# Kernel optimization log

Hardware: AMD Instinct MI355X
Metric: run time of the kernel (lower is better)

## Reference

```python
import jax, jax.numpy as jnp
import numpy as np

C = 256

def setup_inputs() -> dict:
    key = jax.random.key(0)
    ks = jax.random.split(key, 9)
    B, H, W = 32, 32, 32
    s = C ** -0.5  # init scale for weights
    inputs = jax.random.normal(ks[0], (B, H, W, C), jnp.float32)
    Wq = jax.random.normal(ks[1], (C, C), jnp.float32) * s
    Wk = jax.random.normal(ks[2], (C, C), jnp.float32) * s
    Wv = jax.random.normal(ks[3], (C, C), jnp.float32) * s
    Wo = jax.random.normal(ks[4], (C, C), jnp.float32) * s
    bq = jnp.zeros((C,), jnp.float32)
    bk = jnp.zeros((C,), jnp.float32)
    bv = jnp.zeros((C,), jnp.float32)
    bo = jnp.zeros((C,), jnp.float32)
    return {"inputs": inputs, "Wq": Wq, "bq": bq, "Wk": Wk, "bk": bk,
            "Wv": Wv, "bv": bv, "Wo": Wo, "bo": bo}

def reference(inputs, Wq, bq, Wk, bk, Wv, bv, Wo, bo):
    B, H, W, c = inputs.shape
    scale = jnp.float32(c) ** -0.5
    x = inputs.reshape(B, H * W, c)           # 1x1 conv == per-pixel matmul
    q = x @ Wq + bq                           # [B, HW, C]
    k = x @ Wk + bk
    v = x @ Wv + bv
    scores = jnp.einsum('bnc,bmc->bnm', q, k) * scale  # [B, HW, HW]
    attn = jax.nn.softmax(scores, axis=-1)
    attended = jnp.einsum('bnm,bmc->bnc', attn, v)     # [B, HW, C]
    out = attended @ Wo + bo
    return out.reshape(B, H, W, c)
```

## Files before the change

kernel.cpp:

```cpp
#include <hip/hip_runtime.h>
#include <hip/hip_bf16.h>

typedef __bf16 bf16;
typedef __bf16 bf16x2 __attribute__((ext_vector_type(2)));
typedef __bf16 bf16x4 __attribute__((ext_vector_type(4)));
typedef __bf16 bf16x8 __attribute__((ext_vector_type(8)));
typedef float f32x4 __attribute__((ext_vector_type(4)));

#define SM_C 0.09016994374947424f

typedef __attribute__((address_space(1))) const void as1_void;
typedef __attribute__((address_space(3))) void as3_void;

__global__ __launch_bounds__(256) void transpose_w(
    const float* __restrict__ Wq, const float* __restrict__ Wk,
    const float* __restrict__ Wv, const float* __restrict__ Wo,
    bf16* __restrict__ Wt)
{
    __shared__ float T[32][33];
    const int bid = blockIdx.x;
    const int m = bid >> 6, tile = bid & 63;
    const int tn0 = (tile >> 3) * 32, tk0 = (tile & 7) * 32;
    const float* W = (m == 0) ? Wq : (m == 1) ? Wk : (m == 2) ? Wv : Wo;

    const int t = threadIdx.x;
    const int r = t >> 3, c4 = (t & 7) * 4;

    f32x4 v = *(const f32x4*)(W + (size_t)(tk0 + r) * 256 + tn0 + c4);
#pragma unroll
    for (int j = 0; j < 4; ++j) T[r][c4 + j] = v[j];
    __syncthreads();

    bf16x4 ov;
#pragma unroll
    for (int j = 0; j < 4; ++j) ov[j] = (bf16)T[c4 + j][r];
    *(bf16x4*)(Wt + (size_t)m * 65536 + (size_t)(tn0 + r) * 256 + tk0 + c4) = ov;
}

__global__ __launch_bounds__(256, 3) void qkv_gemm(
    const float* __restrict__ X, const bf16* __restrict__ Wt,
    const float* __restrict__ bq, const float* __restrict__ bk,
    const float* __restrict__ bv,
    bf16* __restrict__ Qo, bf16* __restrict__ Ko, bf16* __restrict__ Vto)
{
    __shared__ bf16 Xs[128 * 72];
    __shared__ bf16 Ws_[128 * 72];

    const int t    = threadIdx.x;
    const int lane = t & 63, wv = t >> 6;
    const int quad = lane >> 4, l16 = lane & 15;
    const int bm   = blockIdx.x;
    const int bn   = blockIdx.y;
    const int proj = bn >> 1;

    const bf16* W = Wt + (size_t)proj * 65536 + (size_t)(bn & 1) * 32768;
    const float* bias = (proj == 0) ? bq : (proj == 1) ? bk : bv;

    const int m0 = t >> 3;
    const int c0 = (t & 7) * 8;

    const f32x4 zero = {0.0f, 0.0f, 0.0f, 0.0f};
    f32x4 acc[2][8];
#pragma unroll
    for (int i = 0; i < 2; ++i)
#pragma unroll
        for (int j = 0; j < 8; ++j) acc[i][j] = zero;

    f32x4 xa[4], xb[4]; bf16x8 wp[4];
#pragma unroll
    for (int p = 0; p < 4; ++p) {
        const float* px = X + (size_t)(bm * 128 + m0 + p * 32) * 256 + c0;
        xa[p] = *(const f32x4*)px; xb[p] = *(const f32x4*)(px + 4);
        wp[p] = *(const bf16x8*)(W + (size_t)(m0 + p * 32) * 256 + c0);
    }

    for (int kt = 0; kt < 4; ++kt) {
#pragma unroll
        for (int p = 0; p < 4; ++p) {
            bf16x8 r;
#pragma unroll
            for (int j = 0; j < 4; ++j) { r[j] = (bf16)xa[p][j]; r[j + 4] = (bf16)xb[p][j]; }
            *(bf16x8*)(Xs + (m0 + p * 32) * 72 + c0) = r;
            *(bf16x8*)(Ws_ + (m0 + p * 32) * 72 + c0) = wp[p];
        }
        __syncthreads();

        if (kt < 3) {
#pragma unroll
            for (int p = 0; p < 4; ++p) {
                const float* px = X + (size_t)(bm * 128 + m0 + p * 32) * 256 + (kt + 1) * 64 + c0;
                xa[p] = *(const f32x4*)px; xb[p] = *(const f32x4*)(px + 4);
                wp[p] = *(const bf16x8*)(W + (size_t)(m0 + p * 32) * 256 + (kt + 1) * 64 + c0);
            }
        }

#pragma unroll
        for (int ks = 0; ks < 2; ++ks) {
            bf16x8 a[2], bb[8];
#pragma unroll
            for (int mt = 0; mt < 2; ++mt)
                a[mt] = *(const bf16x8*)(Xs + (wv * 32 + mt * 16 + l16) * 72 + ks * 32 + quad * 8);
#pragma unroll
            for (int nt = 0; nt < 8; ++nt)
                bb[nt] = *(const bf16x8*)(Ws_ + (nt * 16 + l16) * 72 + ks * 32 + quad * 8);
#pragma unroll
            for (int mt = 0; mt < 2; ++mt)
#pragma unroll
                for (int nt = 0; nt < 8; ++nt)
                    acc[mt][nt] = __builtin_amdgcn_mfma_f32_16x16x32_bf16(
                        a[mt], bb[nt], acc[mt][nt], 0, 0, 0);
        }
        __syncthreads();
    }

#pragma unroll
    for (int nt = 0; nt < 8; ++nt) {
        int col = (bn & 1) * 128 + nt * 16 + l16;
        float bvv = bias[col];
#pragma unroll
        for (int mt = 0; mt < 2; ++mt) {
            int grow0 = bm * 128 + wv * 32 + mt * 16 + quad * 4;
            if (proj == 2) {
                bf16x4 pk;
#pragma unroll
                for (int r = 0; r < 4; ++r) pk[r] = (bf16)(acc[mt][nt][r] + bvv);
                int b = grow0 >> 10, m = grow0 & 1023;
                *(bf16x4*)(Vto + (size_t)b * 262144 + (size_t)col * 1024 + m) = pk;
            } else {
                bf16* dst = (proj == 0) ? Qo : Ko;
#pragma unroll
                for (int r = 0; r < 4; ++r)
                    dst[(size_t)(grow0 + r) * 256 + col] = (bf16)(acc[mt][nt][r] + bvv);
            }
        }
    }
}

__global__ __launch_bounds__(512, 2) void flash_attn(
    const bf16* __restrict__ Qr, const bf16* __restrict__ K,
    const bf16* __restrict__ Vt, const bf16* __restrict__ Wo,
    const float* __restrict__ bo, float* __restrict__ out)
{
    __shared__ __align__(16) char smem[155648];

    const int t    = threadIdx.x;
    const int lane = t & 63, wv = t >> 6;
    const int quad = lane >> 4, l16 = lane & 15;
    const int g    = wv >> 2, wl = wv & 3;
    const int gt   = t & 255;
    const int b  = blockIdx.x;
    const int qt = blockIdx.y;

    char* const KsB = smem + g * 73728;
    char* const VsB = smem + g * 73728 + 32768;
    char* const Pb  = smem + 147456 + wv * 1024;
    const int psw = (l16 & 7) << 4;

    bf16x8 qf[2][8];
#pragma unroll
    for (int mt = 0; mt < 2; ++mt) {
        const bf16* qp = Qr + ((size_t)b * 1024 + qt * 128 + wl * 32 + mt * 16 + l16) * 256 + quad * 8;
#pragma unroll
        for (int ks = 0; ks < 8; ++ks)
            qf[mt][ks] = *(const bf16x8*)(qp + ks * 32);
    }

    const f32x4 zero = {0.0f, 0.0f, 0.0f, 0.0f};
    f32x4 o[2][16];
#pragma unroll
    for (int mt = 0; mt < 2; ++mt)
#pragma unroll
        for (int n = 0; n < 16; ++n) o[mt][n] = zero;
    float lst[2] = {0.f, 0.f};

    const int vc  = gt >> 1;
    const int vk8 = (gt & 1) * 8;
    bf16x8 vp[4];

    auto gloadK = [&](int T, int buf) {
#pragma unroll
        for (int p = 0; p < 4; ++p) {
            int chunk = wl * 4 + p;
            int row   = chunk * 2 + (lane >> 5);
            int w16   = (lane & 31) ^ (row & 7);
            const bf16* gsrc = K + ((size_t)b * 1024 + T * 32 + row) * 256 + w16 * 8;
            __builtin_amdgcn_global_load_lds((as1_void*)gsrc,
                (as3_void*)(KsB + buf * 16384 + chunk * 1024), 16, 0, 0);
        }
    };
    auto vload = [&](int T) {
#pragma unroll
        for (int p = 0; p < 4; ++p) {
            int c = vc + 128 * (p >> 1), k8 = vk8 + (p & 1) * 16;
            vp[p] = *(const bf16x8*)(Vt + (size_t)b * 262144 + (size_t)c * 1024 + T * 32 + k8);
        }
    };
    auto vcommit = [&](int buf) {
#pragma unroll
        for (int p = 0; p < 4; ++p) {
            int c = vc + 128 * (p >> 1), k8 = vk8 + (p & 1) * 16;
            *(bf16x8*)(VsB + buf * 20480 + c * 80 + k8 * 2) = vp[p];
        }
    };

    gloadK(g, 0);
    vload(g); vcommit(0); vload(g + 2);

    for (int i = 0; i < 16; ++i) {
        const int buf = i & 1;
        __syncthreads();

        if (i < 15) {
            gloadK(g + 2 * (i + 1), buf ^ 1);
            vcommit(buf ^ 1);
            if (i < 14) vload(g + 2 * (i + 2));
        }

        f32x4 s[2][2];
        s[0][0] = zero; s[0][1] = zero; s[1][0] = zero; s[1][1] = zero;
        const char* Kbuf = KsB + buf * 16384;
#pragma unroll
        for (int ks = 0; ks < 8; ++ks) {
#pragma unroll
            for (int n = 0; n < 2; ++n) {
                bf16x8 kb = *(const bf16x8*)(Kbuf + (n * 16 + l16) * 512 + ((ks * 64 + quad * 16) ^ psw));
                s[0][n] = __builtin_amdgcn_mfma_f32_16x16x32_bf16(kb, qf[0][ks], s[0][n], 0, 0, 0);
                s[1][n] = __builtin_amdgcn_mfma_f32_16x16x32_bf16(kb, qf[1][ks], s[1][n], 0, 0, 0);
            }
        }

        bf16x8 af[2];
#pragma unroll
        for (int mt = 0; mt < 2; ++mt) {
#pragma unroll
            for (int n = 0; n < 2; ++n) {
#pragma unroll
                for (int h = 0; h < 2; ++h) {
                    float p0 = __builtin_amdgcn_exp2f(s[mt][n][2 * h] * SM_C);
                    float p1 = __builtin_amdgcn_exp2f(s[mt][n][2 * h + 1] * SM_C);
                    lst[mt] += p0 + p1;
                    bf16x2 pk; pk[0] = (bf16)p0; pk[1] = (bf16)p1;
                    *(bf16x2*)(Pb + ((l16 * 64 + n * 32 + quad * 8 + h * 4) ^ psw)) = pk;
                }
            }
            af[mt] = *(const bf16x8*)(Pb + ((l16 * 64 + quad * 16) ^ psw));
        }

        const char* Vbuf = VsB + buf * 20480;
#pragma unroll
        for (int n = 0; n < 16; ++n) {
            bf16x8 vb = *(const bf16x8*)(Vbuf + (n * 16 + l16) * 80 + quad * 16);
            o[0][n] = __builtin_amdgcn_mfma_f32_16x16x32_bf16(af[0], vb, o[0][n], 0, 0, 0);
            o[1][n] = __builtin_amdgcn_mfma_f32_16x16x32_bf16(af[1], vb, o[1][n], 0, 0, 0);
        }
    }

    __syncthreads();

#pragma unroll
    for (int mt = 0; mt < 2; ++mt) {
        lst[mt] += __shfl_xor(lst[mt], 16, 64);
        lst[mt] += __shfl_xor(lst[mt], 32, 64);
    }

    float* const scr  = (float*)(smem + 67584);
    float* const lstS = (float*)(smem + 135168);
    bf16*  const Os   = (bf16*)smem;

    if (g == 1) {
        if (quad == 0) {
            lstS[wl * 32 + l16]      = lst[0];
            lstS[wl * 32 + 16 + l16] = lst[1];
        }
#pragma unroll
        for (int mt = 0; mt < 2; ++mt)
#pragma unroll
            for (int n = 0; n < 8; ++n)
                *(f32x4*)(scr + (size_t)(n * 16 + l16) * 132 + wl * 32 + mt * 16 + quad * 4) = o[mt][n];
    }
    __syncthreads();
    if (g == 0) {
        lst[0] += lstS[wl * 32 + l16];
        lst[1] += lstS[wl * 32 + 16 + l16];
#pragma unroll
        for (int mt = 0; mt < 2; ++mt)
#pragma unroll
            for (int n = 0; n < 8; ++n) {
                f32x4 m = *(const f32x4*)(scr + (size_t)(n * 16 + l16) * 132 + wl * 32 + mt * 16 + quad * 4);
                o[mt][n] += m;
            }
    }
    __syncthreads();
    if (g == 1) {
#pragma unroll
        for (int mt = 0; mt < 2; ++mt)
#pragma unroll
            for (int n = 8; n < 16; ++n)
                *(f32x4*)(scr + (size_t)((n - 8) * 16 + l16) * 132 + wl * 32 + mt * 16 + quad * 4) = o[mt][n];
    }
    __syncthreads();
    if (g == 0) {
#pragma unroll
        for (int mt = 0; mt < 2; ++mt)
#pragma unroll
            for (int n = 8; n < 16; ++n) {
                f32x4 m = *(const f32x4*)(scr + (size_t)((n - 8) * 16 + l16) * 132 + wl * 32 + mt * 16 + quad * 4);
                o[mt][n] += m;
            }
        float inv[2][4];
#pragma unroll
        for (int mt = 0; mt < 2; ++mt)
#pragma unroll
            for (int r = 0; r < 4; ++r)
                inv[mt][r] = 1.0f / __shfl(lst[mt], quad * 4 + r, 64);
#pragma unroll
        for (int mt = 0; mt < 2; ++mt)
#pragma unroll
            for (int n = 0; n < 16; ++n)
#pragma unroll
                for (int r = 0; r < 4; ++r)
                    Os[(size_t)(wl * 32 + mt * 16 + quad * 4 + r) * 264 + n * 16 + l16] =
                        (bf16)(o[mt][n][r] * inv[mt][r]);
    }
    __syncthreads();

    bf16* const Wos = (bf16*)(smem + 67584);
    const int rh = (wv & 1) * 64;
    const int nq = wv >> 1;
    const size_t orow0 = (size_t)b * 1024 + qt * 128 + rh;

#pragma unroll
    for (int h = 0; h < 2; ++h) {
        if (h) __syncthreads();
#pragma unroll
        for (int i = 0; i < 8; ++i) {
            int c = t + i * 512;
            int row = c >> 5, c8 = (c & 31) * 8;
            *(bf16x8*)(Wos + row * 264 + c8) =
                *(const bf16x8*)(Wo + (size_t)(h * 128 + row) * 256 + c8);
        }
        __syncthreads();

        f32x4 acc[4][2];
#pragma unroll
        for (int mt = 0; mt < 4; ++mt) { acc[mt][0] = zero; acc[mt][1] = zero; }

#pragma unroll
        for (int ks = 0; ks < 8; ++ks) {
            bf16x8 a[4], bb[2];
#pragma unroll
            for (int mt = 0; mt < 4; ++mt)
                a[mt] = *(const bf16x8*)(Os + (size_t)(rh + mt * 16 + l16) * 264 + ks * 32 + quad * 8);
#pragma unroll
            for (int nt = 0; nt < 2; ++nt)
                bb[nt] = *(const bf16x8*)(Wos + (nq * 32 + nt * 16 + l16) * 264 + ks * 32 + quad * 8);
#pragma unroll
            for (int mt = 0; mt < 4; ++mt)
#pragma unroll
                for (int nt = 0; nt < 2; ++nt)
                    acc[mt][nt] = __builtin_amdgcn_mfma_f32_16x16x32_bf16(
                        a[mt], bb[nt], acc[mt][nt], 0, 0, 0);
        }

#pragma unroll
        for (int nt = 0; nt < 2; ++nt) {
            int col = h * 128 + nq * 32 + nt * 16 + l16;
            float bvv = bo[col];
#pragma unroll
            for (int mt = 0; mt < 4; ++mt) {
#pragma unroll
                for (int r = 0; r < 4; ++r) {
                    size_t row = orow0 + mt * 16 + quad * 4 + r;
                    out[row * 256 + col] = acc[mt][nt][r] + bvv;
                }
            }
        }
    }
}

extern "C" void kernel_launch(void* const* d_in, const int* in_sizes, int n_in,
                              void* d_out, int out_size, void* d_ws, size_t ws_size,
                              hipStream_t stream)
{
    (void)in_sizes; (void)n_in; (void)out_size; (void)ws_size;
    const float* X  = (const float*)d_in[0];
    const float* Wq = (const float*)d_in[1];
    const float* bq = (const float*)d_in[2];
    const float* Wk = (const float*)d_in[3];
    const float* bk = (const float*)d_in[4];
    const float* Wv = (const float*)d_in[5];
    const float* bv = (const float*)d_in[6];
    const float* Wo = (const float*)d_in[7];
    const float* bo = (const float*)d_in[8];
    float* out = (float*)d_out;

    const size_t NTOK = (size_t)32768 * 256;

    bf16* Wt  = (bf16*)d_ws;
    bf16* Qw  = (bf16*)d_ws + 262144;
    bf16* Kw  = Qw + NTOK;
    bf16* Vtw = Kw + NTOK;

    transpose_w<<<256, 256, 0, stream>>>(Wq, Wk, Wv, Wo, Wt);
    qkv_gemm   <<<dim3(256, 6), 256, 0, stream>>>(X, Wt, bq, bk, bv, Qw, Kw, Vtw);
    flash_attn <<<dim3(32, 8),  512, 0, stream>>>(Qw, Kw, Vtw, Wt + 3 * 65536, bo, out);
}
```

Measured before the change: 199.7 us.

## Stage Q/K epilogue through LDS for coalesced stores and remap GEMM blocks per XCD

The QKV GEMM now writes Q and K tiles into shared memory first, then stores them to global memory as coalesced 16-byte vectors instead of scattered 2-byte writes. The grid becomes 1D, and block indices are remapped so that the six column tiles sharing an X row tile land on the same XCD, which should improve L2 reuse of X. The flash_attn launch bound is relaxed from 2 to 1 blocks per CU, giving the compiler more registers at the possible cost of occupancy. The extra LDS staging adds a barrier and reuses the input tile buffers.

```diff
diff --git a/kernel.cpp b/kernel.cpp
--- a/kernel.cpp
+++ b/kernel.cpp
@@ -43,14 +43,19 @@
     const float* __restrict__ bv,
     bf16* __restrict__ Qo, bf16* __restrict__ Ko, bf16* __restrict__ Vto)
 {
-    __shared__ bf16 Xs[128 * 72];
-    __shared__ bf16 Ws_[128 * 72];
+    __shared__ __align__(16) char qsmem[36864];
+    bf16* const Xs  = (bf16*)qsmem;
+    bf16* const Ws_ = (bf16*)(qsmem + 18432);
+    bf16* const Cs  = (bf16*)qsmem;
 
     const int t    = threadIdx.x;
     const int lane = t & 63, wv = t >> 6;
     const int quad = lane >> 4, l16 = lane & 15;
-    const int bm   = blockIdx.x;
-    const int bn   = blockIdx.y;
+
+    const int wg   = blockIdx.x;
+    const int xcd  = wg & 7, slot = wg >> 3;
+    const int bm   = (slot / 6) * 8 + xcd;
+    const int bn   = slot % 6;
     const int proj = bn >> 1;
 
     const bf16* W = Wt + (size_t)proj * 65536 + (size_t)(bn & 1) * 32768;
@@ -113,30 +118,45 @@
         __syncthreads();
     }
 
-#pragma unroll
-    for (int nt = 0; nt < 8; ++nt) {
-        int col = (bn & 1) * 128 + nt * 16 + l16;
-        float bvv = bias[col];
-#pragma unroll
-        for (int mt = 0; mt < 2; ++mt) {
-            int grow0 = bm * 128 + wv * 32 + mt * 16 + quad * 4;
-            if (proj == 2) {
+    if (proj == 2) {
+#pragma unroll
+        for (int nt = 0; nt < 8; ++nt) {
+            int col = (bn & 1) * 128 + nt * 16 + l16;
+            float bvv = bias[col];
+#pragma unroll
+            for (int mt = 0; mt < 2; ++mt) {
+                int grow0 = bm * 128 + wv * 32 + mt * 16 + quad * 4;
                 bf16x4 pk;
 #pragma unroll
                 for (int r = 0; r < 4; ++r) pk[r] = (bf16)(acc[mt][nt][r] + bvv);
                 int b = grow0 >> 10, m = grow0 & 1023;
                 *(bf16x4*)(Vto + (size_t)b * 262144 + (size_t)col * 1024 + m) = pk;
-            } else {
-                bf16* dst = (proj == 0) ? Qo : Ko;
+            }
+        }
+    } else {
+        bf16* dst = (proj == 0) ? Qo : Ko;
+#pragma unroll
+        for (int nt = 0; nt < 8; ++nt) {
+            float bvv = bias[(bn & 1) * 128 + nt * 16 + l16];
+#pragma unroll
+            for (int mt = 0; mt < 2; ++mt)
 #pragma unroll
                 for (int r = 0; r < 4; ++r)
-                    dst[(size_t)(grow0 + r) * 256 + col] = (bf16)(acc[mt][nt][r] + bvv);
-            }
+                    Cs[(wv * 32 + mt * 16 + quad * 4 + r) * 132 + nt * 16 + l16] =
+                        (bf16)(acc[mt][nt][r] + bvv);
+        }
+        __syncthreads();
+#pragma unroll
+        for (int i = 0; i < 8; ++i) {
+            int chunk = i * 256 + t;
+            int row = chunk >> 4, cc = chunk & 15;
+            bf16x8 v = *(const bf16x8*)(Cs + row * 132 + cc * 8);
+            *(bf16x8*)(dst + (size_t)(bm * 128 + row) * 256 + (bn & 1) * 128 + cc * 8) = v;
         }
     }
 }
 
-__global__ __launch_bounds__(512, 2) void flash_attn(
+__global__ __launch_bounds__(512, 1) void flash_attn(
     const bf16* __restrict__ Qr, const bf16* __restrict__ K,
     const bf16* __restrict__ Vt, const bf16* __restrict__ Wo,
     const float* __restrict__ bo, float* __restrict__ out)
@@ -402,6 +422,6 @@
     bf16* Vtw = Kw + NTOK;
 
     transpose_w<<<256, 256, 0, stream>>>(Wq, Wk, Wv, Wo, Wt);
-    qkv_gemm   <<<dim3(256, 6), 256, 0, stream>>>(X, Wt, bq, bk, bv, Qw, Kw, Vtw);
-    flash_attn <<<dim3(32, 8),  512, 0, stream>>>(Qw, Kw, Vtw, Wt + 3 * 65536, bo, out);
+    qkv_gemm   <<<1536, 256, 0, stream>>>(X, Wt, bq, bk, bv, Qw, Kw, Vtw);
+    flash_attn <<<dim3(32, 8), 512, 0, stream>>>(Qw, Kw, Vtw, Wt + 3 * 65536, bo, out);
 }
```

Result: faster. 194.6 us (-2.5%).
